# Optimization experiments

Measured on AMD Instinct MI355X. Metric: run time of the kernel, lower is better.

## Reference

```python
import jax, jax.numpy as jnp
import numpy as np

D_MODEL = 512
NUM_HEADS = 8
D_K = D_MODEL // NUM_HEADS


def setup_inputs() -> dict:
    key = jax.random.key(0)
    ks = jax.random.split(key, 9)
    B, T = 4, 2048
    s = 1.0 / np.sqrt(D_MODEL)
    inp = {"x": jax.random.normal(ks[0], (B, T, D_MODEL), dtype=jnp.float32)}
    names = ["wq", "wk", "wv", "wo"]
    for i, n in enumerate(names):
        inp[n] = jax.random.uniform(ks[1 + i], (D_MODEL, D_MODEL), dtype=jnp.float32, minval=-s, maxval=s)
        inp["b" + n[1]] = jax.random.uniform(ks[5 + i], (D_MODEL,), dtype=jnp.float32, minval=-s, maxval=s)
    return inp


def reference(x, wq, bq, wk, bk, wv, bv, wo, bo):
    B, T, C = x.shape
    # Linear projections (torch Linear: x @ W^T + b)
    q = x @ wq.T + bq
    k = x @ wk.T + bk
    v = x @ wv.T + bv
    # [B, H, T, d_k]
    q = q.reshape(B, T, NUM_HEADS, D_K).transpose(0, 2, 1, 3)
    k = k.reshape(B, T, NUM_HEADS, D_K).transpose(0, 2, 1, 3)
    v = v.reshape(B, T, NUM_HEADS, D_K).transpose(0, 2, 1, 3)
    # scaled dot-product attention, full [B,H,T,T] scores materialized (faithful)
    scores = jnp.einsum('bhqd,bhkd->bhqk', q, k) / jnp.sqrt(jnp.float32(D_K))
    weights = jax.nn.softmax(scores, axis=-1)
    attn = jnp.einsum('bhqk,bhkd->bhqd', weights, v)
    attn = attn.transpose(0, 2, 1, 3).reshape(B, T, C)
    return attn @ wo.T + bo
```

## Files before the change

kernel.cpp:

```cpp
#include <hip/hip_runtime.h>

typedef __bf16 bf16x8 __attribute__((ext_vector_type(8)));
typedef __bf16 bf16x4 __attribute__((ext_vector_type(4)));
typedef float f32x4 __attribute__((ext_vector_type(4)));
typedef float f32x16 __attribute__((ext_vector_type(16)));

#define MFMA_16x16x32(a, b, c) __builtin_amdgcn_mfma_f32_16x16x32_bf16((a), (b), (c), 0, 0, 0)
#define MFMA32(a, b, c) __builtin_amdgcn_mfma_f32_32x32x16_bf16((a), (b), (c), 0, 0, 0)

#define WAIT_LGKM0() do { \
    asm volatile("s_waitcnt lgkmcnt(0)" ::: "memory"); \
    __builtin_amdgcn_sched_barrier(0); } while (0)

typedef const __attribute__((address_space(1))) void GVp;
typedef __attribute__((address_space(3))) void LVp;
#define GLOAD16(gp, lp) \
    __builtin_amdgcn_global_load_lds((GVp*)(gp), (LVp*)(lp), 16, 0, 0)

__device__ __forceinline__ float fexp2(float x) {
    float r;
    asm("v_exp_f32 %0, %1" : "=v"(r) : "v"(x));
    return r;
}

__device__ __forceinline__ unsigned cvtpk(float lo, float hi) {
    unsigned r;
    asm("v_cvt_pk_bf16_f32 %0, %1, %2" : "=v"(r) : "v"(lo), "v"(hi));
    return r;
}
#define PSWAP(a, b) asm volatile("v_permlane32_swap_b32 %0, %1" : "+v"(a), "+v"(b))

union PB { unsigned u[4]; bf16x8 v; };

__device__ __forceinline__ int swz(int row, int colb) {
    return row * 128 + (colb ^ ((row & 7) << 4));
}

__global__ __launch_bounds__(256) void cvt_all(const float* __restrict__ x,
                                               const float* __restrict__ w0,
                                               const float* __restrict__ w1,
                                               const float* __restrict__ w2,
                                               const float* __restrict__ w3,
                                               __bf16* __restrict__ xo,
                                               __bf16* __restrict__ o0,
                                               __bf16* __restrict__ o1,
                                               __bf16* __restrict__ o2,
                                               __bf16* __restrict__ o3) {
    int i = blockIdx.x * 256 + threadIdx.x;
    const float* in;
    __bf16* out;
    int idx;
    if (i < 1048576) {
        in = x; out = xo; idx = i;
    } else {
        int j = i - 1048576;
        int s = j >> 16;
        idx = j & 65535;
        in = (s == 0) ? w0 : (s == 1) ? w1 : (s == 2) ? w2 : w3;
        out = (s == 0) ? o0 : (s == 1) ? o1 : (s == 2) ? o2 : o3;
    }
    float4 v = ((const float4*)in)[idx];
    bf16x4 o;
    o[0] = (__bf16)v.x; o[1] = (__bf16)v.y; o[2] = (__bf16)v.z; o[3] = (__bf16)v.w;
    ((bf16x4*)out)[idx] = o;
}

template <typename OT, bool VT, int BM, int BN>
__device__ __forceinline__ void gemm_body(const __bf16* __restrict__ A,
                                          const __bf16* __restrict__ Bw,
                                          const float* __restrict__ bias,
                                          OT* __restrict__ C,
                                          int K, int N, float scale) {
    const int m0 = blockIdx.x * BM;
    const int n0 = blockIdx.y * BN;
    const int tid = threadIdx.x;
    const int l = tid & 63, w = tid >> 6;
    constexpr int MI = BM / 32;
    constexpr int NI = BN / 32;
    const int wr = w >> 1, wc = w & 1;
    const int lr = l & 15;
    const int lkb = (l >> 4) << 4;

    __shared__ __bf16 As[BM * 64];
    __shared__ __bf16 Bs[BN * 64];
    char* AsC = (char*)As;
    char* BsC = (char*)Bs;

    const int srow = tid >> 3;
    const int c8 = ((tid & 7) ^ (srow & 7)) * 8;

    f32x4 acc[MI][NI] = {};

    for (int k0 = 0; k0 < K; k0 += 64) {
        __syncthreads();
#pragma unroll
        for (int p = 0; p < BM / 32; ++p)
            GLOAD16(A + (size_t)(m0 + p * 32 + srow) * K + k0 + c8,
                    AsC + p * 4096 + tid * 16);
#pragma unroll
        for (int p = 0; p < BN / 32; ++p)
            GLOAD16(Bw + (size_t)(n0 + p * 32 + srow) * K + k0 + c8,
                    BsC + p * 4096 + tid * 16);
        __syncthreads();
#pragma unroll
        for (int kk = 0; kk < 2; ++kk) {
            bf16x8 af[MI], bfr[NI];
#pragma unroll
            for (int mi = 0; mi < MI; ++mi)
                af[mi] = *(const bf16x8*)(AsC + swz(wr * (BM / 2) + mi * 16 + lr, kk * 64 + lkb));
#pragma unroll
            for (int ni = 0; ni < NI; ++ni)
                bfr[ni] = *(const bf16x8*)(BsC + swz(wc * (BN / 2) + ni * 16 + lr, kk * 64 + lkb));
#pragma unroll
            for (int mi = 0; mi < MI; ++mi)
#pragma unroll
                for (int ni = 0; ni < NI; ++ni)
                    acc[mi][ni] = MFMA_16x16x32(af[mi], bfr[ni], acc[mi][ni]);
        }
    }

    const int rb = (l >> 4) * 4;
#pragma unroll
    for (int mi = 0; mi < MI; ++mi) {
#pragma unroll
        for (int ni = 0; ni < NI; ++ni) {
            int gn = n0 + wc * (BN / 2) + ni * 16 + lr;
            int gm = m0 + wr * (BM / 2) + mi * 16 + rb;
            float bv = bias[gn];
            if constexpr (VT) {
                bf16x4 o4;
#pragma unroll
                for (int j = 0; j < 4; ++j)
                    o4[j] = (__bf16)((acc[mi][ni][j] + bv) * scale);
                *(bf16x4*)((__bf16*)C + ((size_t)(gm >> 11) << 20) +
                           (size_t)gn * 2048 + (gm & 2047)) = o4;
            } else {
#pragma unroll
                for (int j = 0; j < 4; ++j) {
                    float v = (acc[mi][ni][j] + bv) * scale;
                    C[(size_t)(gm + j) * N + gn] = (OT)v;
                }
            }
        }
    }
}

#define QSCALE 0.18033688f

__global__ __launch_bounds__(256) void qkv_gemm(const __bf16* __restrict__ X,
                                                const __bf16* __restrict__ Wq,
                                                const __bf16* __restrict__ Wk,
                                                const __bf16* __restrict__ Wv,
                                                const float* __restrict__ bq,
                                                const float* __restrict__ bk,
                                                const float* __restrict__ bv,
                                                __bf16* __restrict__ Qo,
                                                __bf16* __restrict__ Ko,
                                                __bf16* __restrict__ Vto) {
    int z = blockIdx.z;
    if (z == 0) {
        gemm_body<__bf16, false, 64, 128>(X, Wq, bq, Qo, 512, 512, QSCALE);
    } else if (z == 1) {
        gemm_body<__bf16, false, 64, 128>(X, Wk, bk, Ko, 512, 512, 1.0f);
    } else {
        gemm_body<__bf16, true, 64, 128>(X, Wv, bv, Vto, 512, 512, 1.0f);
    }
}

__global__ __launch_bounds__(256) void out_gemm_fused(const __bf16* __restrict__ Op0,
                                                      const __bf16* __restrict__ Op1,
                                                      const float* __restrict__ lsum,
                                                      const __bf16* __restrict__ W,
                                                      const float* __restrict__ bias,
                                                      float* __restrict__ C) {
    const int m0 = blockIdx.x * 64;
    const int n0 = blockIdx.y * 128;
    const int tid = threadIdx.x;
    const int l = tid & 63, w = tid >> 6;
    const int wr = w >> 1, wc = w & 1;
    const int lr = l & 15;
    const int lkb = (l >> 4) << 4;

    __shared__ __bf16 As[64 * 64];
    __shared__ __bf16 Bs[128 * 64];
    __shared__ float2 wts[8][64];
    char* AsC = (char*)As;
    char* BsC = (char*)Bs;

    const int b = m0 >> 11, q0 = m0 & 2047;

#pragma unroll
    for (int j = 0; j < 2; ++j) {
        int idx = tid + j * 256;
        int i = idx & 63, hh = idx >> 6;
        size_t r = (size_t)(b * 8 + hh) * 2048 + q0 + i;
        float l0v = lsum[r], l1v = lsum[65536 + r];
        float inv = 1.f / (l0v + l1v);
        wts[hh][i] = make_float2(l0v * inv, l1v * inv);
    }

    const int srow = tid >> 3;
    const int c8 = ((tid & 7) ^ (srow & 7)) * 8;

    f32x4 acc[2][4] = {};

    for (int k0 = 0; k0 < 512; k0 += 64) {
        __syncthreads();
        const int hh = k0 >> 6;
#pragma unroll
        for (int p = 0; p < 2; ++p) {
            int row = p * 32 + srow;
            size_t r = (size_t)(b * 8 + hh) * 2048 + q0 + row;
            float2 wt = wts[hh][row];
            bf16x8 o0 = *(const bf16x8*)(Op0 + r * 64 + c8);
            bf16x8 o1 = *(const bf16x8*)(Op1 + r * 64 + c8);
            bf16x8 mg;
#pragma unroll
            for (int jj = 0; jj < 8; ++jj)
                mg[jj] = (__bf16)((float)o0[jj] * wt.x + (float)o1[jj] * wt.y);
            *(bf16x8*)(AsC + p * 4096 + tid * 16) = mg;
        }
#pragma unroll
        for (int p = 0; p < 4; ++p)
            GLOAD16(W + (size_t)(n0 + p * 32 + srow) * 512 + k0 + c8,
                    BsC + p * 4096 + tid * 16);
        __syncthreads();
#pragma unroll
        for (int kk = 0; kk < 2; ++kk) {
            bf16x8 af[2], bfr[4];
#pragma unroll
            for (int mi = 0; mi < 2; ++mi)
                af[mi] = *(const bf16x8*)(AsC + swz(wr * 32 + mi * 16 + lr, kk * 64 + lkb));
#pragma unroll
            for (int ni = 0; ni < 4; ++ni)
                bfr[ni] = *(const bf16x8*)(BsC + swz(wc * 64 + ni * 16 + lr, kk * 64 + lkb));
#pragma unroll
            for (int mi = 0; mi < 2; ++mi)
#pragma unroll
                for (int ni = 0; ni < 4; ++ni)
                    acc[mi][ni] = MFMA_16x16x32(af[mi], bfr[ni], acc[mi][ni]);
        }
    }

    const int rb = (l >> 4) * 4;
#pragma unroll
    for (int mi = 0; mi < 2; ++mi) {
#pragma unroll
        for (int ni = 0; ni < 4; ++ni) {
            int gn = n0 + wc * 64 + ni * 16 + lr;
            int gm = m0 + wr * 32 + mi * 16 + rb;
            float bv = bias[gn];
#pragma unroll
            for (int j = 0; j < 4; ++j)
                C[(size_t)(gm + j) * 512 + gn] = acc[mi][ni][j] + bv;
        }
    }
}

__global__ __launch_bounds__(256, 2) void attn_fwd(const __bf16* __restrict__ Q,
                                                   const __bf16* __restrict__ K,
                                                   const __bf16* __restrict__ Vt,
                                                   __bf16* __restrict__ Op0,
                                                   __bf16* __restrict__ Op1,
                                                   float* __restrict__ lsum) {
    const int T = 2048, Cm = 512;
    const int qt0 = blockIdx.x * 256;
    const int h = blockIdx.y;
    const int half = blockIdx.z & 1, b = blockIdx.z >> 1;
    const int kt0 = half * 1024, kend = kt0 + 1024;
    const int tid = threadIdx.x;
    const int l = tid & 63, w = tid >> 6;
    const int q5 = l & 31, hi = l >> 5;
    const size_t rbase = ((size_t)b * T) * Cm + h * 64;
    const size_t vtbase = ((size_t)b << 20) + (size_t)(h * 64) * 2048;

    __shared__ __align__(16) char smem[33792];

    const int grow = tid >> 3;
    const int gcol = ((tid & 7) ^ (grow & 7)) * 8;
    const __bf16* kgp = K + rbase + (size_t)grow * Cm + gcol;
    const __bf16* vgp = Vt + vtbase + (size_t)grow * 2048 + gcol;

#define ATTN_STAGE(nb, ktv)                                                   \
    do {                                                                      \
        char* kd_ = smem + (nb) * 8192 + tid * 16;                            \
        char* vd_ = smem + 16384 + (nb) * 8192 + tid * 16;                    \
        _Pragma("unroll")                                                     \
        for (int p = 0; p < 2; ++p) {                                         \
            GLOAD16(kgp + (size_t)((ktv) + p * 32) * Cm, kd_ + p * 4096);     \
            GLOAD16(vgp + (size_t)(p * 32) * 2048 + (ktv), vd_ + p * 4096);   \
        }                                                                     \
    } while (0)

    bf16x8 qfA[4], qfB[4];
#pragma unroll
    for (int dc = 0; dc < 4; ++dc) {
        qfA[dc] = *(const bf16x8*)(Q + rbase +
            (size_t)(qt0 + w * 64 + q5) * Cm + dc * 16 + hi * 8);
        qfB[dc] = *(const bf16x8*)(Q + rbase +
            (size_t)(qt0 + w * 64 + 32 + q5) * Cm + dc * 16 + hi * 8);
    }

    f32x16 oaA[2] = {}, oaB[2] = {};
    float lA = 0.f, lB = 0.f;

    ATTN_STAGE(0, kt0);
    __syncthreads();

    char* albase = smem + 32768 + w * 256;

    int cur = 0;
    for (int kt = kt0; kt < kend; kt += 64, cur ^= 1) {
        if (kt + 64 < kend) ATTN_STAGE(cur ^ 1, kt + 64);

        const char* kb_ = smem + cur * 8192;
        bf16x8 kf0[4], kf1[4];
#pragma unroll
        for (int dc = 0; dc < 4; ++dc) {
            kf0[dc] = *(const bf16x8*)(kb_ + swz(q5, dc * 32 + hi * 16));
            kf1[dc] = *(const bf16x8*)(kb_ + swz(32 + q5, dc * 32 + hi * 16));
        }

        PB pfA[4], pfB[4];
        {
            f32x16 s0 = {}, s1 = {};
#pragma unroll
            for (int dc = 0; dc < 4; ++dc) {
                __builtin_amdgcn_s_setprio(1);
                s0 = MFMA32(kf0[dc], qfA[dc], s0);
                s1 = MFMA32(kf1[dc], qfA[dc], s1);
                __builtin_amdgcn_s_setprio(0);
            }
            float rs = 0.f;
#pragma unroll
            for (int r = 0; r < 16; ++r) {
                float p0 = fexp2(s0[r]);
                float p1 = fexp2(s1[r]);
                s0[r] = p0; s1[r] = p1;
                rs += p0 + p1;
            }
            rs += __shfl_xor(rs, 32);
            lA += rs;
#pragma unroll
            for (int kb = 0; kb < 2; ++kb) {
#pragma unroll
                for (int cc = 0; cc < 2; ++cc) {
                    int gA = 8 * cc, gB = 8 * cc + 4;
                    float a0, a1, a2, a3, b0, b1, b2, b3;
                    if (kb == 0) {
                        a0 = s0[gA]; a1 = s0[gA + 1]; a2 = s0[gA + 2]; a3 = s0[gA + 3];
                        b0 = s0[gB]; b1 = s0[gB + 1]; b2 = s0[gB + 2]; b3 = s0[gB + 3];
                    } else {
                        a0 = s1[gA]; a1 = s1[gA + 1]; a2 = s1[gA + 2]; a3 = s1[gA + 3];
                        b0 = s1[gB]; b1 = s1[gB + 1]; b2 = s1[gB + 2]; b3 = s1[gB + 3];
                    }
                    unsigned w0A = cvtpk(a0, a1), w1A = cvtpk(a2, a3);
                    unsigned w0B = cvtpk(b0, b1), w1B = cvtpk(b2, b3);
                    PSWAP(w0A, w0B);
                    PSWAP(w1A, w1B);
                    int kc = 2 * kb + cc;
                    pfA[kc].u[0] = w0A; pfA[kc].u[1] = w1A;
                    pfA[kc].u[2] = w0B; pfA[kc].u[3] = w1B;
                }
            }
        }

        {
            f32x16 s0 = {}, s1 = {};
#pragma unroll
            for (int dc = 0; dc < 4; ++dc) {
                __builtin_amdgcn_s_setprio(1);
                s0 = MFMA32(kf0[dc], qfB[dc], s0);
                s1 = MFMA32(kf1[dc], qfB[dc], s1);
                __builtin_amdgcn_s_setprio(0);
            }
            float rs = 0.f;
#pragma unroll
            for (int r = 0; r < 16; ++r) {
                float p0 = fexp2(s0[r]);
                float p1 = fexp2(s1[r]);
                s0[r] = p0; s1[r] = p1;
                rs += p0 + p1;
            }
            rs += __shfl_xor(rs, 32);
            lB += rs;
#pragma unroll
            for (int kb = 0; kb < 2; ++kb) {
#pragma unroll
                for (int cc = 0; cc < 2; ++cc) {
                    int gA = 8 * cc, gB = 8 * cc + 4;
                    float a0, a1, a2, a3, b0, b1, b2, b3;
                    if (kb == 0) {
                        a0 = s0[gA]; a1 = s0[gA + 1]; a2 = s0[gA + 2]; a3 = s0[gA + 3];
                        b0 = s0[gB]; b1 = s0[gB + 1]; b2 = s0[gB + 2]; b3 = s0[gB + 3];
                    } else {
                        a0 = s1[gA]; a1 = s1[gA + 1]; a2 = s1[gA + 2]; a3 = s1[gA + 3];
                        b0 = s1[gB]; b1 = s1[gB + 1]; b2 = s1[gB + 2]; b3 = s1[gB + 3];
                    }
                    unsigned w0A = cvtpk(a0, a1), w1A = cvtpk(a2, a3);
                    unsigned w0B = cvtpk(b0, b1), w1B = cvtpk(b2, b3);
                    PSWAP(w0A, w0B);
                    PSWAP(w1A, w1B);
                    int kc = 2 * kb + cc;
                    pfB[kc].u[0] = w0A; pfB[kc].u[1] = w1A;
                    pfB[kc].u[2] = w0B; pfB[kc].u[3] = w1B;
                }
            }
        }

        const char* vb_ = smem + 16384 + cur * 8192;
#pragma unroll
        for (int kc = 0; kc < 4; ++kc) {
            bf16x8 vf0 = *(const bf16x8*)(vb_ + swz(q5, kc * 32 + hi * 16));
            bf16x8 vf1 = *(const bf16x8*)(vb_ + swz(32 + q5, kc * 32 + hi * 16));
            __builtin_amdgcn_s_setprio(1);
            oaA[0] = MFMA32(pfA[kc].v, vf0, oaA[0]);
            oaA[1] = MFMA32(pfA[kc].v, vf1, oaA[1]);
            oaB[0] = MFMA32(pfB[kc].v, vf0, oaB[0]);
            oaB[1] = MFMA32(pfB[kc].v, vf1, oaB[1]);
            __builtin_amdgcn_s_setprio(0);
        }

        __syncthreads();
    }

    __bf16* Opb = half ? Op1 : Op0;
    const size_t rr = (size_t)(b * 8 + h) * 2048;
    {
        float invl = 1.f / lA;
        *(float*)(albase + q5 * 4) = invl;
        WAIT_LGKM0();
        f32x4 ivr[4];
#pragma unroll
        for (int rg = 0; rg < 4; ++rg)
            ivr[rg] = *(const f32x4*)(albase + hi * 16 + rg * 32);
#pragma unroll
        for (int rg = 0; rg < 4; ++rg)
#pragma unroll
            for (int c = 0; c < 4; ++c) {
                int qr = qt0 + w * 64 + 8 * rg + 4 * hi + c;
                float iv = ivr[rg][c];
                Opb[(rr + qr) * 64 + q5]      = (__bf16)(oaA[0][4 * rg + c] * iv);
                Opb[(rr + qr) * 64 + 32 + q5] = (__bf16)(oaA[1][4 * rg + c] * iv);
            }
    }
    {
        float invl = 1.f / lB;
        *(float*)(albase + 128 + q5 * 4) = invl;
        WAIT_LGKM0();
        f32x4 ivr[4];
#pragma unroll
        for (int rg = 0; rg < 4; ++rg)
            ivr[rg] = *(const f32x4*)(albase + 128 + hi * 16 + rg * 32);
#pragma unroll
        for (int rg = 0; rg < 4; ++rg)
#pragma unroll
            for (int c = 0; c < 4; ++c) {
                int qr = qt0 + w * 64 + 32 + 8 * rg + 4 * hi + c;
                float iv = ivr[rg][c];
                Opb[(rr + qr) * 64 + q5]      = (__bf16)(oaB[0][4 * rg + c] * iv);
                Opb[(rr + qr) * 64 + 32 + q5] = (__bf16)(oaB[1][4 * rg + c] * iv);
            }
    }
    if (hi == 0) {
        lsum[(size_t)half * 65536 + rr + qt0 + w * 64 + q5] = lA;
        lsum[(size_t)half * 65536 + rr + qt0 + w * 64 + 32 + q5] = lB;
    }
#undef ATTN_STAGE
}

extern "C" void kernel_launch(void* const* d_in, const int* in_sizes, int n_in,
                              void* d_out, int out_size, void* d_ws, size_t ws_size,
                              hipStream_t stream) {
    const float* x  = (const float*)d_in[0];
    const float* wq = (const float*)d_in[1];
    const float* bq = (const float*)d_in[2];
    const float* wk = (const float*)d_in[3];
    const float* bk = (const float*)d_in[4];
    const float* wv = (const float*)d_in[5];
    const float* bv = (const float*)d_in[6];
    const float* wo = (const float*)d_in[7];
    const float* bo = (const float*)d_in[8];

    char* ws = (char*)d_ws;
    __bf16* xb    = (__bf16*)(ws);
    __bf16* Op0   = (__bf16*)(ws);
    __bf16* Qb    = (__bf16*)(ws + ((size_t)8 << 20));
    __bf16* Kb    = (__bf16*)(ws + ((size_t)16 << 20));
    __bf16* Vtb   = (__bf16*)(ws + ((size_t)24 << 20));
    __bf16* Op1   = (__bf16*)(ws + ((size_t)32 << 20));
    __bf16* wqb   = (__bf16*)(ws + ((size_t)40 << 20));
    __bf16* wkb   = (__bf16*)(ws + ((size_t)40 << 20) + ((size_t)512 << 10));
    __bf16* wvb   = (__bf16*)(ws + ((size_t)40 << 20) + ((size_t)1024 << 10));
    __bf16* wob   = (__bf16*)(ws + ((size_t)40 << 20) + ((size_t)1536 << 10));
    float*  lsb   = (float*)(ws + ((size_t)42 << 20));

    cvt_all<<<dim3(5120), dim3(256), 0, stream>>>(x, wq, wk, wv, wo,
                                                  xb, wqb, wkb, wvb, wob);
    qkv_gemm<<<dim3(128, 4, 3), dim3(256), 0, stream>>>(xb, wqb, wkb, wvb,
                                                        bq, bk, bv, Qb, Kb, Vtb);
    attn_fwd<<<dim3(8, 8, 8), dim3(256), 0, stream>>>(Qb, Kb, Vtb, Op0, Op1, lsb);
    out_gemm_fused<<<dim3(128, 4), dim3(256), 0, stream>>>(Op0, Op1, lsb, wob, bo,
                                                           (float*)d_out);
}
```

Before: 87.45 us.

## Double-buffer LDS tiles in projection and output GEMMs to overlap loads

Both the shared projection GEMM body and the fused output GEMM now use two LDS buffers per operand. The next K-tile is prefetched while MFMAs run on the current one, and each iteration needs one barrier instead of two. The goal is to hide global-load latency behind compute in the GEMM phases. The cost is double the LDS footprint, which may lower occupancy. Correctness also depends on the global_load_lds completing by the barrier, since no explicit vmcnt wait is issued.

```diff
diff --git a/kernel.cpp b/kernel.cpp
--- a/kernel.cpp
+++ b/kernel.cpp
@@ -77,47 +77,60 @@
     const int l = tid & 63, w = tid >> 6;
     constexpr int MI = BM / 32;
     constexpr int NI = BN / 32;
+    constexpr int ABYTES = BM * 128;
+    constexpr int BBYTES = BN * 128;
     const int wr = w >> 1, wc = w & 1;
     const int lr = l & 15;
     const int lkb = (l >> 4) << 4;
 
-    __shared__ __bf16 As[BM * 64];
-    __shared__ __bf16 Bs[BN * 64];
+    __shared__ __bf16 As[2 * BM * 64];
+    __shared__ __bf16 Bs[2 * BN * 64];
     char* AsC = (char*)As;
     char* BsC = (char*)Bs;
 
     const int srow = tid >> 3;
     const int c8 = ((tid & 7) ^ (srow & 7)) * 8;
 
+#define GEMM_STAGE(nb, k0v)                                                   \
+    do {                                                                      \
+        _Pragma("unroll")                                                     \
+        for (int p = 0; p < BM / 32; ++p)                                     \
+            GLOAD16(A + (size_t)(m0 + p * 32 + srow) * K + (k0v) + c8,        \
+                    AsC + (nb) * ABYTES + p * 4096 + tid * 16);               \
+        _Pragma("unroll")                                                     \
+        for (int p = 0; p < BN / 32; ++p)                                     \
+            GLOAD16(Bw + (size_t)(n0 + p * 32 + srow) * K + (k0v) + c8,       \
+                    BsC + (nb) * BBYTES + p * 4096 + tid * 16);               \
+    } while (0)
+
     f32x4 acc[MI][NI] = {};
 
-    for (int k0 = 0; k0 < K; k0 += 64) {
-        __syncthreads();
-#pragma unroll
-        for (int p = 0; p < BM / 32; ++p)
-            GLOAD16(A + (size_t)(m0 + p * 32 + srow) * K + k0 + c8,
-                    AsC + p * 4096 + tid * 16);
-#pragma unroll
-        for (int p = 0; p < BN / 32; ++p)
-            GLOAD16(Bw + (size_t)(n0 + p * 32 + srow) * K + k0 + c8,
-                    BsC + p * 4096 + tid * 16);
-        __syncthreads();
+    GEMM_STAGE(0, 0);
+    __syncthreads();
+
+    int cur = 0;
+    for (int k0 = 0; k0 < K; k0 += 64, cur ^= 1) {
+        if (k0 + 64 < K) GEMM_STAGE(cur ^ 1, k0 + 64);
+        const char* Ab = AsC + cur * ABYTES;
+        const char* Bb = BsC + cur * BBYTES;
 #pragma unroll
         for (int kk = 0; kk < 2; ++kk) {
             bf16x8 af[MI], bfr[NI];
 #pragma unroll
             for (int mi = 0; mi < MI; ++mi)
-                af[mi] = *(const bf16x8*)(AsC + swz(wr * (BM / 2) + mi * 16 + lr, kk * 64 + lkb));
+                af[mi] = *(const bf16x8*)(Ab + swz(wr * (BM / 2) + mi * 16 + lr, kk * 64 + lkb));
 #pragma unroll
             for (int ni = 0; ni < NI; ++ni)
-                bfr[ni] = *(const bf16x8*)(BsC + swz(wc * (BN / 2) + ni * 16 + lr, kk * 64 + lkb));
+                bfr[ni] = *(const bf16x8*)(Bb + swz(wc * (BN / 2) + ni * 16 + lr, kk * 64 + lkb));
 #pragma unroll
             for (int mi = 0; mi < MI; ++mi)
 #pragma unroll
                 for (int ni = 0; ni < NI; ++ni)
                     acc[mi][ni] = MFMA_16x16x32(af[mi], bfr[ni], acc[mi][ni]);
         }
-    }
+        __syncthreads();
+    }
+#undef GEMM_STAGE
 
     const int rb = (l >> 4) * 4;
 #pragma unroll
@@ -181,8 +194,8 @@
     const int lr = l & 15;
     const int lkb = (l >> 4) << 4;
 
-    __shared__ __bf16 As[64 * 64];
-    __shared__ __bf16 Bs[128 * 64];
+    __shared__ __bf16 As[2 * 64 * 64];
+    __shared__ __bf16 Bs[2 * 128 * 64];
     __shared__ float2 wts[8][64];
     char* AsC = (char*)As;
     char* BsC = (char*)Bs;
@@ -198,49 +211,61 @@
         float inv = 1.f / (l0v + l1v);
         wts[hh][i] = make_float2(l0v * inv, l1v * inv);
     }
+    __syncthreads();
 
     const int srow = tid >> 3;
     const int c8 = ((tid & 7) ^ (srow & 7)) * 8;
 
+#define OUT_STAGE(nb, hh)                                                     \
+    do {                                                                      \
+        _Pragma("unroll")                                                     \
+        for (int p = 0; p < 2; ++p) {                                         \
+            int row = p * 32 + srow;                                          \
+            size_t r = (size_t)(b * 8 + (hh)) * 2048 + q0 + row;              \
+            float2 wt = wts[hh][row];                                         \
+            bf16x8 o0 = *(const bf16x8*)(Op0 + r * 64 + c8);                  \
+            bf16x8 o1 = *(const bf16x8*)(Op1 + r * 64 + c8);                  \
+            bf16x8 mg;                                                        \
+            _Pragma("unroll")                                                 \
+            for (int jj = 0; jj < 8; ++jj)                                    \
+                mg[jj] = (__bf16)((float)o0[jj] * wt.x + (float)o1[jj] * wt.y); \
+            *(bf16x8*)(AsC + (nb) * 8192 + p * 4096 + tid * 16) = mg;         \
+        }                                                                     \
+        _Pragma("unroll")                                                     \
+        for (int p = 0; p < 4; ++p)                                           \
+            GLOAD16(W + (size_t)(n0 + p * 32 + srow) * 512 + (hh) * 64 + c8,  \
+                    BsC + (nb) * 16384 + p * 4096 + tid * 16);                \
+    } while (0)
+
     f32x4 acc[2][4] = {};
 
-    for (int k0 = 0; k0 < 512; k0 += 64) {
-        __syncthreads();
+    OUT_STAGE(0, 0);
+    __syncthreads();
+
+    int cur = 0;
+    for (int k0 = 0; k0 < 512; k0 += 64, cur ^= 1) {
         const int hh = k0 >> 6;
-#pragma unroll
-        for (int p = 0; p < 2; ++p) {
-            int row = p * 32 + srow;
-            size_t r = (size_t)(b * 8 + hh) * 2048 + q0 + row;
-            float2 wt = wts[hh][row];
-            bf16x8 o0 = *(const bf16x8*)(Op0 + r * 64 + c8);
-            bf16x8 o1 = *(const bf16x8*)(Op1 + r * 64 + c8);
-            bf16x8 mg;
-#pragma unroll
-            for (int jj = 0; jj < 8; ++jj)
-                mg[jj] = (__bf16)((float)o0[jj] * wt.x + (float)o1[jj] * wt.y);
-            *(bf16x8*)(AsC + p * 4096 + tid * 16) = mg;
-        }
-#pragma unroll
-        for (int p = 0; p < 4; ++p)
-            GLOAD16(W + (size_t)(n0 + p * 32 + srow) * 512 + k0 + c8,
-                    BsC + p * 4096 + tid * 16);
-        __syncthreads();
+        if (hh + 1 < 8) OUT_STAGE(cur ^ 1, hh + 1);
+        const char* Ab = AsC + cur * 8192;
+        const char* Bb = BsC + cur * 16384;
 #pragma unroll
         for (int kk = 0; kk < 2; ++kk) {
             bf16x8 af[2], bfr[4];
 #pragma unroll
             for (int mi = 0; mi < 2; ++mi)
-                af[mi] = *(const bf16x8*)(AsC + swz(wr * 32 + mi * 16 + lr, kk * 64 + lkb));
+                af[mi] = *(const bf16x8*)(Ab + swz(wr * 32 + mi * 16 + lr, kk * 64 + lkb));
 #pragma unroll
             for (int ni = 0; ni < 4; ++ni)
-                bfr[ni] = *(const bf16x8*)(BsC + swz(wc * 64 + ni * 16 + lr, kk * 64 + lkb));
+                bfr[ni] = *(const bf16x8*)(Bb + swz(wc * 64 + ni * 16 + lr, kk * 64 + lkb));
 #pragma unroll
             for (int mi = 0; mi < 2; ++mi)
 #pragma unroll
                 for (int ni = 0; ni < 4; ++ni)
                     acc[mi][ni] = MFMA_16x16x32(af[mi], bfr[ni], acc[mi][ni]);
         }
-    }
+        __syncthreads();
+    }
+#undef OUT_STAGE
 
     const int rb = (l >> 4) * 4;
 #pragma unroll
```

New measurement: 111.3 us. 1.27x slower.
